# Performance work log

Measured on AMD Instinct MI355X. Metric: run time of the kernel, lower is better.

## Reference

```python
import jax, jax.numpy as jnp
from jax import lax
import numpy as np

IOU_TH = 0.5
SCORE_TH = 0.05
MAX_PER_CLASS = 10
MAX_TOTAL = 10
K_PRE = 200  # pre-NMS candidates per class (>> max_output_size_per_class)


def make_anchors(image_size: int) -> jnp.ndarray:
    """Replicates AnchorBoxes.create_anchors_boxes for square images (static shapes)."""
    aspect_ratios = [0.5, 1.0, 2.0]
    scales = [2.0 ** 0, 2.0 ** (1.0 / 3.0), 2.0 ** (2.0 / 3.0)]
    step = (image_size - 32) // 4
    areas = [(x * step + 32) ** 2 for x in range(5)]
    strides = [2 ** i for i in range(3, 8)]
    levels = []
    for l in range(5):
        fs = int(np.ceil(image_size / strides[l]))
        dims = []
        for r in aspect_ratios:  # order matches TF code: ratio outer, scale inner
            h = np.sqrt(areas[l] / r)
            w = areas[l] / h
            for s in scales:
                dims.append([s * w, s * h])
        dims = np.asarray(dims, np.float32)  # [9, 2]
        c = (np.arange(fs, dtype=np.float32) + 0.5) * strides[l]
        X, Y = np.meshgrid(c, c)  # 'xy' indexing, as in tf.meshgrid default
        centers = np.stack([X, Y], -1)  # [fs, fs, 2] (cx, cy)
        centers = np.broadcast_to(centers[:, :, None, :], (fs, fs, 9, 2))
        d = np.broadcast_to(dims[None, None], (fs, fs, 9, 2))
        levels.append(np.concatenate([centers, d], -1).reshape(-1, 4))
    return jnp.asarray(np.concatenate(levels, 0))  # [N, 4] (cx, cy, w, h)


def pairwise_iou(b):  # b: [..., K, 4] in corner format
    lt = jnp.maximum(b[..., :, None, :2], b[..., None, :, :2])
    rb = jnp.minimum(b[..., :, None, 2:], b[..., None, :, 2:])
    wh = jnp.clip(rb - lt, 0.0)
    inter = wh[..., 0] * wh[..., 1]
    area = (b[..., 2] - b[..., 0]) * (b[..., 3] - b[..., 1])
    union = area[..., :, None] + area[..., None, :] - inter
    return inter / jnp.maximum(union, 1e-8)


def setup_inputs() -> dict:
    key = jax.random.key(0)
    k1, k2 = jax.random.split(key)
    images = jax.random.normal(k1, (32, 512, 512, 3), dtype=jnp.float32)
    predictions = jax.random.normal(k2, (32, 49104, 7), dtype=jnp.float32)
    return {"images": images, "predictions": predictions}


def reference(images, predictions):
    B = predictions.shape[0]
    anchors = make_anchors(images.shape[1])  # [N, 4], static shape
    box_var = jnp.asarray([0.1, 0.1, 0.2, 0.2], predictions.dtype)

    # Decode boxes.
    bp = predictions[:, :, :4] * box_var
    cls = jax.nn.sigmoid(predictions[:, :, 4:])  # [B, N, C]
    a = anchors[None]
    xy = bp[..., :2] * a[..., 2:] + a[..., :2]
    wh = jnp.exp(bp[..., 2:]) * a[..., 2:]
    boxes = jnp.concatenate([xy - wh / 2.0, xy + wh / 2.0], -1)  # [B, N, 4] corners

    # Combined NMS (class-aware, shared boxes q=1).
    scores = jnp.transpose(cls, (0, 2, 1))  # [B, C, N]
    C = scores.shape[1]
    top_s, top_i = lax.top_k(scores, K_PRE)  # [B, C, K]
    bK = jnp.take_along_axis(boxes[:, None], top_i[..., None], axis=2)  # [B, C, K, 4]
    iou = pairwise_iou(bK)  # [B, C, K, K]
    valid = top_s >= SCORE_TH
    idx = jnp.arange(K_PRE)

    def body(i, keep):
        alive = keep[..., i][..., None]
        suppress = (iou[..., i, :] > IOU_TH) & alive & (idx > i)
        return keep & ~suppress

    keep = lax.fori_loop(0, K_PRE, body, valid)
    sel = jnp.where(keep, top_s, -1.0)

    pc_s, pc_i = lax.top_k(sel, MAX_PER_CLASS)  # [B, C, 10]
    pc_b = jnp.take_along_axis(bK, pc_i[..., None], axis=2)  # [B, C, 10, 4]
    pc_c = jnp.broadcast_to(jnp.arange(C, dtype=jnp.float32)[None, :, None], pc_s.shape)

    flat_s = pc_s.reshape(B, -1)
    flat_b = pc_b.reshape(B, -1, 4)
    flat_c = pc_c.reshape(B, -1)
    fs, fi = lax.top_k(flat_s, MAX_TOTAL)  # [B, 10]
    fb = jnp.take_along_axis(flat_b, fi[..., None], axis=1)
    fc = jnp.take_along_axis(flat_c, fi, axis=1)

    valid_mask = fs > 0.0
    nmsed_boxes = jnp.where(valid_mask[..., None], fb, 0.0)
    nmsed_scores = jnp.where(valid_mask, fs, 0.0)
    nmsed_classes = jnp.where(valid_mask, fc, 0.0)
    valid_detections = jnp.sum(valid_mask, axis=-1).astype(jnp.int32)
    return nmsed_boxes, nmsed_scores, nmsed_classes, valid_detections
```

## Files before the change

kernel.cpp:

```cpp
#include <hip/hip_runtime.h>
#include <math.h>

#define NA      49104
#define NB      32
#define KPRE    200
#define CAP     2048
#define NSLICE  64
#define NQ4     85932
#define PERQ    1344
#define STHR    448
#define TAU     2.0f
#define NBINS   512
#define SLOTCAP 64
#define NTHR    1024

#define WS_CNT   0
#define WS_KEYS  24576
#define WS_S10   (WS_KEYS + 96*NSLICE*SLOTCAP*8)
#define WS_B10   (WS_S10 + 96*10*4)
#define WS_DONE  (WS_B10 + 96*10*16)

__device__ __forceinline__ void anchor_of(int idx, float& cx, float& cy,
                                          float& aw, float& ah) {
    int l, r;
    if (idx < 36864)      { l = 0; r = idx; }
    else if (idx < 46080) { l = 1; r = idx - 36864; }
    else if (idx < 48384) { l = 2; r = idx - 46080; }
    else if (idx < 48960) { l = 3; r = idx - 48384; }
    else                  { l = 4; r = idx - 48960; }
    const int   fss[5]     = {64, 32, 16, 8, 4};
    const int   strides[5] = {8, 16, 32, 64, 128};
    const double areas[5]  = {1024.0, 23104.0, 73984.0, 153664.0, 262144.0};
    int a    = r % 9;
    int cell = r / 9;
    int fs   = fss[l];
    int jx   = cell % fs;
    int iy   = cell / fs;
    cx = ((float)jx + 0.5f) * (float)strides[l];
    cy = ((float)iy + 0.5f) * (float)strides[l];
    int ri = a / 3, si = a % 3;
    double ratio = (ri == 0) ? 0.5 : ((ri == 1) ? 1.0 : 2.0);
    double h = sqrt(areas[l] / ratio);
    double w = areas[l] / h;
    double s = (si == 0) ? 1.0
             : ((si == 1) ? 1.2599210498948732
                          : 1.5874010519681994);
    aw = (float)(s * w);
    ah = (float)(s * h);
}

__device__ __forceinline__ int bin_of(float x) {
    int bin = (int)floorf((x + 8.0f) * 32.0f);
    return min(max(bin, 0), NBINS - 1);
}

__device__ __forceinline__ unsigned omap(float x) {
    unsigned u = __float_as_uint(x);
    return u ^ ((u >> 31) ? 0xFFFFFFFFu : 0x80000000u);
}

__device__ __forceinline__ unsigned long long shfl_xor_u64(unsigned long long v,
                                                           int m) {
    unsigned lo = (unsigned)v, hi = (unsigned)(v >> 32);
    lo = __shfl_xor(lo, m, 64);
    hi = __shfl_xor(hi, m, 64);
    return ((unsigned long long)hi << 32) | lo;
}

__global__ __launch_bounds__(STHR) void scan_kernel(
        const float* __restrict__ pred, unsigned* __restrict__ cnts,
        unsigned long long* __restrict__ keys, unsigned* __restrict__ done) {
    const int blk = blockIdx.x;
    const int b   = blk >> 6;
    const int sl  = blk & 63;
    const int tid = threadIdx.x;

    __shared__ unsigned long long stage[3][SLOTCAP];
    __shared__ unsigned scnt[3];
    if (tid < 3) scnt[tid] = 0u;
    __syncthreads();

    const int p = tid % 7;
    int cls[4];
    #pragma unroll
    for (int j = 0; j < 4; ++j) {
        int f = (4 * p + j) % 7;
        cls[j] = (f >= 4) ? (f - 4) : -1;
    }

    const float4* row = (const float4*)(pred + (size_t)b * NA * 7);
    const int q0 = sl * PERQ + tid;
    const int q1 = q0 + STHR, q2 = q1 + STHR;
    float4 v0, v1, v2;
    bool g0 = q0 < NQ4, g1 = q1 < NQ4, g2 = q2 < NQ4;
    if (g0) v0 = row[q0];
    if (g1) v1 = row[q1];
    if (g2) v2 = row[q2];

    #pragma unroll
    for (int it = 0; it < 3; ++it) {
        bool   g = (it == 0) ? g0 : (it == 1) ? g1 : g2;
        float4 v = (it == 0) ? v0 : (it == 1) ? v1 : v2;
        int    q = (it == 0) ? q0 : (it == 1) ? q1 : q2;
        if (!g) continue;
        float vv[4] = {v.x, v.y, v.z, v.w};
        #pragma unroll
        for (int j = 0; j < 4; ++j) {
            if (cls[j] >= 0 && vv[j] >= TAU) {
                int e = (q << 2) + j;
                int n = e / 7;
                unsigned u = __float_as_uint(vv[j]) | 0x80000000u;
                unsigned long long key =
                    ((unsigned long long)(~u) << 32) | (unsigned)n;
                int c = cls[j];
                unsigned pos = atomicAdd(&scnt[c], 1u);
                if (pos < SLOTCAP) stage[c][pos] = key;
            }
        }
    }
    __syncthreads();

    if (tid < 3) cnts[(b * 3 + tid) * NSLICE + sl] = scnt[tid];
    if (tid == 3 && sl == 0) done[b] = 0u;

    #pragma unroll
    for (int c = 0; c < 3; ++c) {
        unsigned n = min(scnt[c], (unsigned)SLOTCAP);
        unsigned long long* dst =
            keys + ((size_t)(b * 3 + c) * NSLICE + sl) * SLOTCAP;
        for (unsigned i = tid; i < n; i += STHR) dst[i] = stage[c][i];
    }
}

__device__ __forceinline__ void bitonic_sort(unsigned long long* buf, unsigned P,
                                             int tid) {
    for (unsigned k = 2; k <= P; k <<= 1) {
        for (unsigned j = k >> 1; j > 0; j >>= 1) {
            for (unsigned i = tid; i < P; i += NTHR) {
                unsigned ixj = i ^ j;
                if (ixj > i) {
                    bool up = ((i & k) == 0);
                    unsigned long long a = buf[i], bb = buf[ixj];
                    if ((a > bb) == up) { buf[i] = bb; buf[ixj] = a; }
                }
            }
            __syncthreads();
        }
    }
}

__global__ __launch_bounds__(NTHR) void nms_merge_kernel(
        const float* __restrict__ pred, const unsigned* __restrict__ cnts,
        const unsigned long long* __restrict__ gkeys,
        float* __restrict__ s10, float4* __restrict__ b10,
        unsigned* __restrict__ done, float* __restrict__ out) {
    const int blk = blockIdx.x;
    const int tid = threadIdx.x;

    if (blk >= 96) {
        const int b = blk - 96;
        if (tid == 0) {
            while (__hip_atomic_load(&done[b], __ATOMIC_ACQUIRE,
                                     __HIP_MEMORY_SCOPE_AGENT) < 3u)
                __builtin_amdgcn_s_sleep(8);
        }
        __syncthreads();
        __threadfence();

        if (tid < 64) {
            float s = (tid < 30) ? s10[b * 30 + tid] : -2.0f;
            float* ob = out + b * 40;
            float* os = out + 1280 + b * 10;
            float* oc = out + 1600 + b * 10;
            float* ov = out + 1920 + b;
            int valid = 0;
            for (int k = 0; k < 10; ++k) {
                unsigned u = __float_as_uint(s);
                unsigned o = (u >> 31) ? ~u : (u | 0x80000000u);
                unsigned long long key =
                    ((unsigned long long)o << 6) | (unsigned)(63 - tid);
                #pragma unroll
                for (int off = 1; off < 64; off <<= 1) {
                    unsigned long long k2 = __shfl_xor(key, off, 64);
                    key = (k2 > key) ? k2 : key;
                }
                int t = 63 - (int)(key & 63ULL);
                float best = __shfl(s, t, 64);
                bool v = best > 0.0f;
                if (tid == t) {
                    float4 bb = v ? b10[b * 30 + t] : make_float4(0, 0, 0, 0);
                    ob[k * 4 + 0] = bb.x; ob[k * 4 + 1] = bb.y;
                    ob[k * 4 + 2] = bb.z; ob[k * 4 + 3] = bb.w;
                    os[k] = v ? best : 0.0f;
                    oc[k] = v ? (float)(t / 10) : 0.0f;
                    s = -2.0f;
                }
                valid += v ? 1 : 0;
            }
            if (tid == 0) ov[0] = (float)valid;
        }
        return;
    }

    const int b = blk / 3;
    const int c = blk % 3;

    __shared__ unsigned long long keybuf[CAP];
    __shared__ unsigned long long sortbuf[512];
    __shared__ float4 boxes[KPRE];
    __shared__ float  scores_s[256];
    __shared__ unsigned long long mask[256][4];
    __shared__ unsigned hist[256];
    __shared__ unsigned hist512[NBINS];
    __shared__ unsigned Lb[NSLICE], Bb[NSLICE];
    __shared__ unsigned sMn[16], sMx[16];
    __shared__ unsigned sel_thr, sel_cnt, s_prefB, s_cumB, s_M, s_sh, s_common;
    __shared__ int sT;

    if (tid < 256) hist[tid] = 0u;
    if (tid == 0) sel_cnt = 0u;

    if (tid < 64) {
        unsigned L  = cnts[blk * NSLICE + tid];
        unsigned Lc = min(L, (unsigned)SLOTCAP);
        unsigned pre = Lc;
        #pragma unroll
        for (int off = 1; off < 64; off <<= 1) {
            unsigned v = __shfl_up(pre, off, 64);
            if (tid >= off) pre += v;
        }
        Lb[tid] = Lc;
        Bb[tid] = pre - Lc;
        unsigned long long ob = __ballot(L > SLOTCAP);
        if (tid == 63) s_M = pre;
        if (tid == 0)  s_common = (ob == 0ULL) ? 1u : 0u;
    }
    __syncthreads();

    const unsigned M0 = s_M;
    const bool common = s_common && M0 >= KPRE && M0 <= CAP;

    if (common) {
        const unsigned long long* src = gkeys + (size_t)blk * NSLICE * SLOTCAP;
        #pragma unroll
        for (int u = 0; u < NSLICE * SLOTCAP / NTHR; ++u) {
            int i = u * NTHR + tid;
            int sl = i >> 6, k = i & (SLOTCAP - 1);
            if ((unsigned)k < Lb[sl]) keybuf[Bb[sl] + k] = src[i];
        }
    } else {
        for (int i = tid; i < NBINS; i += NTHR) hist512[i] = 0u;
        if (tid == 0) s_M = 0u;
        __syncthreads();
        const float* base = pred + (size_t)b * NA * 7 + 4 + c;
        for (int n = tid; n < NA; n += NTHR)
            atomicAdd(&hist512[bin_of(base[(size_t)n * 7])], 1u);
        __syncthreads();
        if (tid < 64) {
            unsigned h[8]; unsigned lsum = 0;
            #pragma unroll
            for (int k = 0; k < 8; ++k) { h[k] = hist512[tid*8+k]; lsum += h[k]; }
            unsigned suf = lsum;
            #pragma unroll
            for (int off = 1; off < 64; off <<= 1) {
                unsigned v = __shfl_down(suf, off, 64);
                if (tid < 64 - off) suf += v;
            }
            unsigned acc = suf - lsum;
            #pragma unroll
            for (int k = 7; k >= 0; --k) {
                unsigned na = acc + h[k];
                if (na >= KPRE && acc < KPRE) sT = max(tid*8 + k - 1, 0);
                acc = na;
            }
        }
        __syncthreads();
        const int T = sT;
        for (int n = tid; n < NA; n += NTHR) {
            float x = base[(size_t)n * 7];
            if (bin_of(x) >= T) {
                unsigned long long key =
                    ((unsigned long long)(~omap(x)) << 32) | (unsigned)n;
                unsigned pos = atomicAdd(&s_M, 1u);
                if (pos < CAP) keybuf[pos] = key;
            }
        }
    }
    __syncthreads();
    const unsigned M = min(s_M, (unsigned)CAP);

    if (M > KPRE) {
        {
            unsigned mn = 0xFFu, mx = 0u;
            for (int i = tid; i < (int)M; i += NTHR) {
                unsigned h = (unsigned)(keybuf[i] >> 56);
                mn = min(mn, h); mx = max(mx, h);
            }
            #pragma unroll
            for (int off = 1; off < 64; off <<= 1) {
                mn = min(mn, (unsigned)__shfl_xor((int)mn, off, 64));
                mx = max(mx, (unsigned)__shfl_xor((int)mx, off, 64));
            }
            if ((tid & 63) == 0) { sMn[tid >> 6] = mn; sMx[tid >> 6] = mx; }
        }
        __syncthreads();
        if (tid == 0) {
            unsigned mn = 0xFFu, mx = 0u;
            #pragma unroll
            for (int w = 0; w < NTHR / 64; ++w) {
                mn = min(mn, sMn[w]); mx = max(mx, sMx[w]);
            }
            s_sh = (mn == mx) ? 40u : 48u;
        }
        __syncthreads();
        const unsigned sh = s_sh;

        for (int i = tid; i < (int)M; i += NTHR)
            atomicAdd(&hist[(unsigned)(keybuf[i] >> (sh + 8)) & 0xFFu], 1u);
        __syncthreads();
        if (tid < 64) {
            unsigned h0 = hist[tid*4],   h1 = hist[tid*4+1];
            unsigned h2 = hist[tid*4+2], h3 = hist[tid*4+3];
            unsigned lsum = h0 + h1 + h2 + h3;
            unsigned pre = lsum;
            #pragma unroll
            for (int off = 1; off < 64; off <<= 1) {
                unsigned v = __shfl_up(pre, off, 64);
                if (tid >= off) pre += v;
            }
            unsigned acc = pre - lsum;
            if (acc < KPRE) {
                if      (acc + h0            >= KPRE) { s_prefB = tid*4;   s_cumB = acc; }
                else if (acc + h0 + h1       >= KPRE) { s_prefB = tid*4+1; s_cumB = acc+h0; }
                else if (acc + h0 + h1 + h2  >= KPRE) { s_prefB = tid*4+2; s_cumB = acc+h0+h1; }
                else if (acc + lsum          >= KPRE) { s_prefB = tid*4+3; s_cumB = acc+h0+h1+h2; }
            }
        }
        __syncthreads();
        const unsigned B = s_prefB, before = s_cumB;
        if (tid < 256) hist[tid] = 0u;
        __syncthreads();
        for (int i = tid; i < (int)M; i += NTHR) {
            unsigned long long key = keybuf[i];
            if (((unsigned)(key >> (sh + 8)) & 0xFFu) == B)
                atomicAdd(&hist[(unsigned)(key >> sh) & 0xFFu], 1u);
        }
        __syncthreads();
        if (tid < 64) {
            const unsigned target = KPRE - before;
            unsigned h0 = hist[tid*4],   h1 = hist[tid*4+1];
            unsigned h2 = hist[tid*4+2], h3 = hist[tid*4+3];
            unsigned lsum = h0 + h1 + h2 + h3;
            unsigned pre = lsum;
            #pragma unroll
            for (int off = 1; off < 64; off <<= 1) {
                unsigned v = __shfl_up(pre, off, 64);
                if (tid >= off) pre += v;
            }
            unsigned acc = pre - lsum;
            if (acc < target) {
                unsigned b2 = 256;
                if      (acc + h0           >= target) b2 = tid*4;
                else if (acc + h0 + h1      >= target) b2 = tid*4+1;
                else if (acc + h0 + h1 + h2 >= target) b2 = tid*4+2;
                else if (acc + lsum         >= target) b2 = tid*4+3;
                if (b2 < 256) sel_thr = (B << 8) | b2;
            }
        }
        __syncthreads();
        const unsigned thr = sel_thr;
        for (int i = tid; i < (int)M; i += NTHR) {
            unsigned long long key = keybuf[i];
            if (((unsigned)(key >> sh) & 0xFFFFu) <= thr) {
                unsigned pos = atomicAdd(&sel_cnt, 1u);
                if (pos < 512) sortbuf[pos] = key;
            }
        }
        __syncthreads();
    } else {
        for (int i = tid; i < (int)M; i += NTHR) sortbuf[i] = keybuf[i];
        if (tid == 0) sel_cnt = M;
        __syncthreads();
    }

    const unsigned C2 = sel_cnt;
    unsigned long long* sorted;
    if (C2 <= 256) {
        unsigned long long v = ~0ULL;
        if (tid < 256) {
            v = (tid < (int)C2) ? sortbuf[tid] : ~0ULL;
            #pragma unroll
            for (unsigned k = 2; k <= 64; k <<= 1) {
                for (unsigned j = k >> 1; j > 0; j >>= 1) {
                    unsigned long long o = shfl_xor_u64(v, (int)j);
                    bool tm = (((tid & k) == 0) == ((tid & j) == 0));
                    v = tm ? (v < o ? v : o) : (v > o ? v : o);
                }
            }
        }
        __syncthreads();
        if (tid < 256) sortbuf[tid] = v;
        __syncthreads();
        if (tid < 256) {
            unsigned long long o = sortbuf[tid ^ 64];
            bool tm = (((tid & 128) == 0) == ((tid & 64) == 0));
            v = tm ? (v < o ? v : o) : (v > o ? v : o);
            #pragma unroll
            for (unsigned j = 32; j > 0; j >>= 1) {
                unsigned long long o2 = shfl_xor_u64(v, (int)j);
                bool t2 = (((tid & 128) == 0) == ((tid & j) == 0));
                v = t2 ? (v < o2 ? v : o2) : (v > o2 ? v : o2);
            }
        }
        __syncthreads();
        if (tid < 256) sortbuf[tid] = v;
        __syncthreads();
        if (tid < 256) {
            unsigned long long o = sortbuf[tid ^ 128];
            bool tm = ((tid & 128) == 0);
            v = tm ? (v < o ? v : o) : (v > o ? v : o);
        }
        __syncthreads();
        if (tid < 256) sortbuf[tid] = v;
        __syncthreads();
        if (tid < 256) {
            unsigned long long o = sortbuf[tid ^ 64];
            bool tm = ((tid & 64) == 0);
            v = tm ? (v < o ? v : o) : (v > o ? v : o);
            #pragma unroll
            for (unsigned j = 32; j > 0; j >>= 1) {
                unsigned long long o2 = shfl_xor_u64(v, (int)j);
                bool t2 = ((tid & j) == 0);
                v = t2 ? (v < o2 ? v : o2) : (v > o2 ? v : o2);
            }
        }
        __syncthreads();
        if (tid < 256) sortbuf[tid] = v;
        __syncthreads();
        sorted = sortbuf;
    } else if (C2 <= 512) {
        for (int i = (int)C2 + tid; i < 512; i += NTHR) sortbuf[i] = ~0ULL;
        __syncthreads();
        bitonic_sort(sortbuf, 512, tid);
        sorted = sortbuf;
    } else {
        for (int i = (int)M + tid; i < CAP; i += NTHR) keybuf[i] = ~0ULL;
        __syncthreads();
        bitonic_sort(keybuf, CAP, tid);
        sorted = keybuf;
    }

    if (tid < KPRE) {
        unsigned long long key = sorted[tid];
        if (key != ~0ULL) {
            unsigned n = (unsigned)key;
            unsigned v = ~(unsigned)(key >> 32);
            v = (v >> 31) ? (v ^ 0x80000000u) : ~v;
            float x  = __uint_as_float(v);
            float sc = 1.0f / (1.0f + expf(-x));
            const float* bp = pred + (size_t)b * NA * 7 + (size_t)n * 7;
            float d0 = bp[0] * 0.1f, d1 = bp[1] * 0.1f;
            float d2 = bp[2] * 0.2f, d3 = bp[3] * 0.2f;
            float cx, cy, aw, ah;
            anchor_of((int)n, cx, cy, aw, ah);
            float xx = d0 * aw + cx;
            float yy = d1 * ah + cy;
            float ww = expf(d2) * aw;
            float hh = expf(d3) * ah;
            boxes[tid]    = make_float4(xx - ww * 0.5f, yy - hh * 0.5f,
                                        xx + ww * 0.5f, yy + hh * 0.5f);
            scores_s[tid] = sc;
        } else {
            boxes[tid]    = make_float4(0, 0, 0, 0);
            scores_s[tid] = -1.0f;
        }
    } else if (tid < 256) {
        scores_s[tid] = -1.0f;
    }
    __syncthreads();

    {
        const int row = tid & 255;
        const int cb  = tid >> 8;
        unsigned long long m = 0ULL;
        if (row < KPRE) {
            const int lo = cb * 64;
            const int hi = min(lo + 64, KPRE);
            float4 bi = boxes[row];
            float areai = (bi.z - bi.x) * (bi.w - bi.y);
            for (int j = max(row + 1, lo); j < hi; ++j) {
                float4 bj = boxes[j];
                float x1 = fmaxf(bi.x, bj.x), y1 = fmaxf(bi.y, bj.y);
                float x2 = fminf(bi.z, bj.z), y2 = fminf(bi.w, bj.w);
                float iw = fmaxf(x2 - x1, 0.0f), ih = fmaxf(y2 - y1, 0.0f);
                float inter = iw * ih;
                float areaj = (bj.z - bj.x) * (bj.w - bj.y);
                float uni   = fmaxf(areai + areaj - inter, 1e-8f);
                if (inter / uni > 0.5f) m |= 1ULL << (j - lo);
            }
        }
        mask[row][cb] = m;
    }
    __syncthreads();

    if (tid < 64) {
        const int lane = tid;
        unsigned long long keep[4];
        #pragma unroll
        for (int cb = 0; cb < 4; ++cb)
            keep[cb] = __ballot(scores_s[cb * 64 + lane] >= 0.05f);

        #pragma unroll
        for (int cb = 0; cb < 4; ++cb) {
            unsigned long long mw_self = mask[cb * 64 + lane][cb];
            unsigned long long kw   = keep[cb];
            unsigned long long work = kw & __ballot(mw_self != 0ULL);
            while (work) {
                int t = __ffsll(work) - 1;
                work &= work - 1;
                if ((kw >> t) & 1ULL) {
                    unsigned long long m = __shfl(mw_self, t, 64);
                    kw   &= ~m;
                    work &= ~m;
                }
            }
            keep[cb] = kw;
            #pragma unroll
            for (int w = cb + 1; w < 4; ++w) {
                unsigned long long myw = mask[cb * 64 + lane][w];
                if ((__ballot(myw != 0ULL) & kw) == 0ULL) continue;
                unsigned long long contrib = ((kw >> lane) & 1ULL) ? myw : 0ULL;
                #pragma unroll
                for (int off = 1; off < 64; off <<= 1)
                    contrib |= __shfl_xor(contrib, off, 64);
                keep[w] &= ~contrib;
            }
        }

        if (lane == 0) {
            int k = 0;
            #pragma unroll
            for (int cb = 0; cb < 4; ++cb) {
                unsigned long long kw = keep[cb];
                while (kw && k < 10) {
                    int t = __ffsll(kw) - 1; kw &= kw - 1;
                    int i = cb * 64 + t;
                    s10[blk * 10 + k] = scores_s[i];
                    b10[blk * 10 + k] = boxes[i];
                    ++k;
                }
            }
            #pragma unroll
            for (int cb = 0; cb < 4; ++cb) {
                unsigned long long nk = ~keep[cb];
                if (cb == 3) nk &= 0xFFULL;
                while (nk && k < 10) {
                    int t = __ffsll(nk) - 1; nk &= nk - 1;
                    int i = cb * 64 + t;
                    s10[blk * 10 + k] = -1.0f;
                    b10[blk * 10 + k] = boxes[i];
                    ++k;
                }
            }
            __threadfence();
            __hip_atomic_fetch_add(&done[b], 1u, __ATOMIC_RELEASE,
                                   __HIP_MEMORY_SCOPE_AGENT);
        }
    }
}

extern "C" void kernel_launch(void* const* d_in, const int* in_sizes, int n_in,
                              void* d_out, int out_size, void* d_ws, size_t ws_size,
                              hipStream_t stream) {
    const float* pred = (const float*)d_in[1];

    char* ws = (char*)d_ws;
    unsigned*            cnts = (unsigned*)           (ws + WS_CNT);
    unsigned long long*  keys = (unsigned long long*) (ws + WS_KEYS);
    float*               s10  = (float*)              (ws + WS_S10);
    float4*              b10  = (float4*)             (ws + WS_B10);
    unsigned*            done = (unsigned*)           (ws + WS_DONE);

    scan_kernel     <<<NB * NSLICE, STHR, 0, stream>>>(pred, cnts, keys, done);
    nms_merge_kernel<<<128, NTHR, 0, stream>>>(pred, cnts, keys, s10, b10, done,
                                               (float*)d_out);
}
```

Before: 57.04 us.

## Fuse candidate scan into NMS kernel with per-class strided column reads

```diff
diff --git a/kernel.cpp b/kernel.cpp
--- a/kernel.cpp
+++ b/kernel.cpp
@@ -5,20 +5,14 @@
 #define NB      32
 #define KPRE    200
 #define CAP     2048
-#define NSLICE  64
-#define NQ4     85932
-#define PERQ    1344
-#define STHR    448
 #define TAU     2.0f
 #define NBINS   512
-#define SLOTCAP 64
 #define NTHR    1024
-
-#define WS_CNT   0
-#define WS_KEYS  24576
-#define WS_S10   (WS_KEYS + 96*NSLICE*SLOTCAP*8)
-#define WS_B10   (WS_S10 + 96*10*4)
-#define WS_DONE  (WS_B10 + 96*10*16)
+#define NITER   48
+
+#define WS_DONE  0
+#define WS_S10   128
+#define WS_B10   (WS_S10 + 3840)
 
 __device__ __forceinline__ void anchor_of(int idx, float& cx, float& cy,
                                           float& aw, float& ah) {
@@ -67,71 +61,6 @@
     return ((unsigned long long)hi << 32) | lo;
 }
 
-__global__ __launch_bounds__(STHR) void scan_kernel(
-        const float* __restrict__ pred, unsigned* __restrict__ cnts,
-        unsigned long long* __restrict__ keys, unsigned* __restrict__ done) {
-    const int blk = blockIdx.x;
-    const int b   = blk >> 6;
-    const int sl  = blk & 63;
-    const int tid = threadIdx.x;
-
-    __shared__ unsigned long long stage[3][SLOTCAP];
-    __shared__ unsigned scnt[3];
-    if (tid < 3) scnt[tid] = 0u;
-    __syncthreads();
-
-    const int p = tid % 7;
-    int cls[4];
-    #pragma unroll
-    for (int j = 0; j < 4; ++j) {
-        int f = (4 * p + j) % 7;
-        cls[j] = (f >= 4) ? (f - 4) : -1;
-    }
-
-    const float4* row = (const float4*)(pred + (size_t)b * NA * 7);
-    const int q0 = sl * PERQ + tid;
-    const int q1 = q0 + STHR, q2 = q1 + STHR;
-    float4 v0, v1, v2;
-    bool g0 = q0 < NQ4, g1 = q1 < NQ4, g2 = q2 < NQ4;
-    if (g0) v0 = row[q0];
-    if (g1) v1 = row[q1];
-    if (g2) v2 = row[q2];
-
-    #pragma unroll
-    for (int it = 0; it < 3; ++it) {
-        bool   g = (it == 0) ? g0 : (it == 1) ? g1 : g2;
-        float4 v = (it == 0) ? v0 : (it == 1) ? v1 : v2;
-        int    q = (it == 0) ? q0 : (it == 1) ? q1 : q2;
-        if (!g) continue;
-        float vv[4] = {v.x, v.y, v.z, v.w};
-        #pragma unroll
-        for (int j = 0; j < 4; ++j) {
-            if (cls[j] >= 0 && vv[j] >= TAU) {
-                int e = (q << 2) + j;
-                int n = e / 7;
-                unsigned u = __float_as_uint(vv[j]) | 0x80000000u;
-                unsigned long long key =
-                    ((unsigned long long)(~u) << 32) | (unsigned)n;
-                int c = cls[j];
-                unsigned pos = atomicAdd(&scnt[c], 1u);
-                if (pos < SLOTCAP) stage[c][pos] = key;
-            }
-        }
-    }
-    __syncthreads();
-
-    if (tid < 3) cnts[(b * 3 + tid) * NSLICE + sl] = scnt[tid];
-    if (tid == 3 && sl == 0) done[b] = 0u;
-
-    #pragma unroll
-    for (int c = 0; c < 3; ++c) {
-        unsigned n = min(scnt[c], (unsigned)SLOTCAP);
-        unsigned long long* dst =
-            keys + ((size_t)(b * 3 + c) * NSLICE + sl) * SLOTCAP;
-        for (unsigned i = tid; i < n; i += STHR) dst[i] = stage[c][i];
-    }
-}
-
 __device__ __forceinline__ void bitonic_sort(unsigned long long* buf, unsigned P,
                                              int tid) {
     for (unsigned k = 2; k <= P; k <<= 1) {
@@ -149,9 +78,8 @@
     }
 }
 
-__global__ __launch_bounds__(NTHR) void nms_merge_kernel(
-        const float* __restrict__ pred, const unsigned* __restrict__ cnts,
-        const unsigned long long* __restrict__ gkeys,
+__global__ __launch_bounds__(NTHR) void fused_kernel(
+        const float* __restrict__ pred,
         float* __restrict__ s10, float4* __restrict__ b10,
         unsigned* __restrict__ done, float* __restrict__ out) {
     const int blk = blockIdx.x;
@@ -204,6 +132,7 @@
 
     const int b = blk / 3;
     const int c = blk % 3;
+    const int lane = tid & 63;
 
     __shared__ unsigned long long keybuf[CAP];
     __shared__ unsigned long long sortbuf[512];
@@ -212,49 +141,46 @@
     __shared__ unsigned long long mask[256][4];
     __shared__ unsigned hist[256];
     __shared__ unsigned hist512[NBINS];
-    __shared__ unsigned Lb[NSLICE], Bb[NSLICE];
     __shared__ unsigned sMn[16], sMx[16];
-    __shared__ unsigned sel_thr, sel_cnt, s_prefB, s_cumB, s_M, s_sh, s_common;
+    __shared__ unsigned sel_thr, sel_cnt, s_prefB, s_cumB, s_M, s_sh;
     __shared__ int sT;
 
     if (tid < 256) hist[tid] = 0u;
-    if (tid == 0) sel_cnt = 0u;
-
-    if (tid < 64) {
-        unsigned L  = cnts[blk * NSLICE + tid];
-        unsigned Lc = min(L, (unsigned)SLOTCAP);
-        unsigned pre = Lc;
-        #pragma unroll
-        for (int off = 1; off < 64; off <<= 1) {
-            unsigned v = __shfl_up(pre, off, 64);
-            if (tid >= off) pre += v;
-        }
-        Lb[tid] = Lc;
-        Bb[tid] = pre - Lc;
-        unsigned long long ob = __ballot(L > SLOTCAP);
-        if (tid == 63) s_M = pre;
-        if (tid == 0)  s_common = (ob == 0ULL) ? 1u : 0u;
-    }
+    if (tid == 0) { sel_cnt = 0u; s_M = 0u; }
     __syncthreads();
 
+    const float* col = pred + (size_t)b * NA * 7 + 4 + c;
+    for (int it = 0; it < NITER; ++it) {
+        int n = it * NTHR + tid;
+        float x = (n < NA) ? col[(size_t)n * 7] : -1e30f;
+        bool ok = (x >= TAU);
+        unsigned long long mb = __ballot(ok);
+        unsigned cnt = (unsigned)__popcll(mb);
+        if (cnt) {
+            unsigned basep = 0;
+            if (lane == 0) basep = atomicAdd(&s_M, cnt);
+            basep = __shfl(basep, 0, 64);
+            if (ok) {
+                unsigned off = (unsigned)__popcll(mb & ((1ULL << lane) - 1ULL));
+                unsigned pos = basep + off;
+                if (pos < CAP) {
+                    unsigned u = __float_as_uint(x) | 0x80000000u;
+                    keybuf[pos] = ((unsigned long long)(~u) << 32) | (unsigned)n;
+                }
+            }
+        }
+    }
+    __syncthreads();
+
     const unsigned M0 = s_M;
-    const bool common = s_common && M0 >= KPRE && M0 <= CAP;
-
-    if (common) {
-        const unsigned long long* src = gkeys + (size_t)blk * NSLICE * SLOTCAP;
-        #pragma unroll
-        for (int u = 0; u < NSLICE * SLOTCAP / NTHR; ++u) {
-            int i = u * NTHR + tid;
-            int sl = i >> 6, k = i & (SLOTCAP - 1);
-            if ((unsigned)k < Lb[sl]) keybuf[Bb[sl] + k] = src[i];
-        }
-    } else {
+    const bool common = (M0 >= KPRE && M0 <= CAP);
+
+    if (!common) {
         for (int i = tid; i < NBINS; i += NTHR) hist512[i] = 0u;
         if (tid == 0) s_M = 0u;
         __syncthreads();
-        const float* base = pred + (size_t)b * NA * 7 + 4 + c;
         for (int n = tid; n < NA; n += NTHR)
-            atomicAdd(&hist512[bin_of(base[(size_t)n * 7])], 1u);
+            atomicAdd(&hist512[bin_of(col[(size_t)n * 7])], 1u);
         __syncthreads();
         if (tid < 64) {
             unsigned h[8]; unsigned lsum = 0;
@@ -276,17 +202,27 @@
         }
         __syncthreads();
         const int T = sT;
-        for (int n = tid; n < NA; n += NTHR) {
-            float x = base[(size_t)n * 7];
-            if (bin_of(x) >= T) {
-                unsigned long long key =
-                    ((unsigned long long)(~omap(x)) << 32) | (unsigned)n;
-                unsigned pos = atomicAdd(&s_M, 1u);
-                if (pos < CAP) keybuf[pos] = key;
-            }
-        }
-    }
-    __syncthreads();
+        for (int it = 0; it < NITER; ++it) {
+            int n = it * NTHR + tid;
+            float x = (n < NA) ? col[(size_t)n * 7] : -1e30f;
+            bool ok = (n < NA) && (bin_of(x) >= T);
+            unsigned long long mb = __ballot(ok);
+            unsigned cnt = (unsigned)__popcll(mb);
+            if (cnt) {
+                unsigned basep = 0;
+                if (lane == 0) basep = atomicAdd(&s_M, cnt);
+                basep = __shfl(basep, 0, 64);
+                if (ok) {
+                    unsigned off = (unsigned)__popcll(mb & ((1ULL << lane) - 1ULL));
+                    unsigned pos = basep + off;
+                    if (pos < CAP)
+                        keybuf[pos] =
+                            ((unsigned long long)(~omap(x)) << 32) | (unsigned)n;
+                }
+            }
+        }
+        __syncthreads();
+    }
     const unsigned M = min(s_M, (unsigned)CAP);
 
     if (M > KPRE) {
@@ -301,7 +237,7 @@
                 mn = min(mn, (unsigned)__shfl_xor((int)mn, off, 64));
                 mx = max(mx, (unsigned)__shfl_xor((int)mx, off, 64));
             }
-            if ((tid & 63) == 0) { sMn[tid >> 6] = mn; sMx[tid >> 6] = mx; }
+            if (lane == 0) { sMn[tid >> 6] = mn; sMx[tid >> 6] = mx; }
         }
         __syncthreads();
         if (tid == 0) {
@@ -504,7 +440,6 @@
     __syncthreads();
 
     if (tid < 64) {
-        const int lane = tid;
         unsigned long long keep[4];
         #pragma unroll
         for (int cb = 0; cb < 4; ++cb)
@@ -575,13 +510,10 @@
     const float* pred = (const float*)d_in[1];
 
     char* ws = (char*)d_ws;
-    unsigned*            cnts = (unsigned*)           (ws + WS_CNT);
-    unsigned long long*  keys = (unsigned long long*) (ws + WS_KEYS);
-    float*               s10  = (float*)              (ws + WS_S10);
-    float4*              b10  = (float4*)             (ws + WS_B10);
-    unsigned*            done = (unsigned*)           (ws + WS_DONE);
-
-    scan_kernel     <<<NB * NSLICE, STHR, 0, stream>>>(pred, cnts, keys, done);
-    nms_merge_kernel<<<128, NTHR, 0, stream>>>(pred, cnts, keys, s10, b10, done,
-                                               (float*)d_out);
-}
+    unsigned* done = (unsigned*)(ws + WS_DONE);
+    float*    s10  = (float*)   (ws + WS_S10);
+    float4*   b10  = (float4*)  (ws + WS_B10);
+
+    hipMemsetAsync(done, 0, NB * sizeof(unsigned), stream);
+    fused_kernel<<<128, NTHR, 0, stream>>>(pred, s10, b10, done, (float*)d_out);
+}
```

Result: slower. 81.03 us (+42.1%).
